# Kernel optimization log

Hardware: AMD Instinct MI355X
Metric: run time of the kernel (lower is better)

The kernel has to match this reference:

```python
import jax, jax.numpy as jnp
import numpy as np

N_NODES = 50000
K_MAX = 10
BATCH = 64
T = 32
N_INPUTS = 16
BITS_PER_FEATURE = 4
INPUT_BITS = N_INPUTS * BITS_PER_FEATURE  # 64


def setup_inputs() -> dict:
    key = jax.random.key(0)
    ks = jax.random.split(key, 8)
    x = jax.random.randint(ks[0], (BATCH, T, INPUT_BITS), 0, 2, dtype=jnp.int32)
    adj_list = jax.random.randint(ks[1], (N_NODES, K_MAX), 0, N_NODES, dtype=jnp.int32)
    adj_list_mask = jax.random.randint(ks[2], (N_NODES, K_MAX), 0, 2, dtype=jnp.int32)
    lut = jax.random.randint(ks[3], (N_NODES, 2 ** K_MAX), 0, 2, dtype=jnp.int32)
    init_states = jax.random.randint(ks[4], (N_NODES,), 0, 2, dtype=jnp.int32)
    input_nodes = jax.random.randint(ks[5], (INPUT_BITS,), 0, N_NODES, dtype=jnp.int32)
    W = jax.random.normal(ks[6], (N_INPUTS, N_NODES), dtype=jnp.float32) * (1.0 / np.sqrt(N_NODES))
    b = jax.random.normal(ks[7], (N_INPUTS,), dtype=jnp.float32) * 0.01
    return {"x": x, "adj_list": adj_list, "adj_list_mask": adj_list_mask,
            "lut": lut, "init_states": init_states, "input_nodes": input_nodes,
            "W": W, "b": b}


def reference(x, adj_list, adj_list_mask, lut, init_states, input_nodes, W, b):
    B, T_, _ = x.shape
    N, K = adj_list.shape
    # powers_of_2 = 2**arange(K).flip()  (MSB-first bit packing)
    pow2 = (2 ** jnp.arange(K - 1, -1, -1)).astype(jnp.int32)  # [K]
    node_ids = jnp.arange(N, dtype=jnp.int32)  # [N]
    s0 = jnp.broadcast_to(init_states[None, :], (B, N)).astype(jnp.int32)

    def step(states, x_t):
        # xor input perturbation at input_nodes
        cur = states[:, input_nodes]                      # [B, INPUT_BITS]
        states = states.at[:, input_nodes].set(jnp.bitwise_xor(cur, x_t))
        # gather masked neighbor states and bit-pack into LUT index
        neigh = jnp.take(states, adj_list, axis=1)        # [B, N, K]
        idx = jnp.sum(neigh * adj_list_mask[None] * pow2, axis=-1)  # [B, N]
        new_states = lut[node_ids[None, :], idx]          # [B, N]
        return new_states, None

    final_states, _ = jax.lax.scan(step, s0, jnp.moveaxis(x, 1, 0))
    # readout = nn.Linear(n_nodes, n_inputs) on final binary states
    out = final_states.astype(jnp.float32) @ W.T + b      # [B, N_INPUTS]
    return out
```

## Files before the change

### kernel.cpp

```cpp
#include <hip/hip_runtime.h>
#include <stdint.h>

#define N_NODES    50000
#define K_MAX      10
#define BATCH      64
#define T_STEPS    32
#define N_INPUTS   16
#define INPUT_BITS 64

#define NPW   256
#define NWG   196
#define NTHR  1024

#define OFF_BUF0   0u
#define OFF_BUF1   400128u
#define OFF_XMASK  800256u
#define OFF_CTR    816640u

__global__ void prep_kernel(const int* __restrict__ x,
                            const int* __restrict__ init_states,
                            const int* __restrict__ input_nodes,
                            uint64_t* __restrict__ buf0,
                            uint64_t* __restrict__ buf1,
                            uint64_t* __restrict__ xmask,
                            uint32_t* __restrict__ ctr) {
    int gid = blockIdx.x * blockDim.x + threadIdx.x;
    if (gid < N_NODES) {
        int n = gid;
        int jm = -1;
        for (int j = 0; j < INPUT_BITS; ++j)
            if (input_nodes[j] == n) jm = j;
        uint64_t v = init_states[n] ? ~0ull : 0ull;
        if (jm >= 0) {
            uint64_t m = 0ull;
            for (int b = 0; b < BATCH; ++b)
                m |= (uint64_t)(x[b * (T_STEPS * INPUT_BITS) + jm] & 1) << b;
            v ^= m;
        }
        buf0[n] = v;
    } else if (gid == N_NODES) {
        buf0[N_NODES] = 0ull; buf1[N_NODES] = 0ull;
    } else if (gid < N_NODES + 1 + T_STEPS * INPUT_BITS) {
        int k = gid - (N_NODES + 1);
        int t = k >> 6, j = k & 63;
        uint64_t m = 0ull;
        for (int b = 0; b < BATCH; ++b)
            m |= (uint64_t)(x[b * (T_STEPS * INPUT_BITS) + t * INPUT_BITS + j] & 1) << b;
        xmask[k] = m;
    } else {
        int c = gid - (N_NODES + 1 + T_STEPS * INPUT_BITS);
        if (c < T_STEPS) ctr[c] = 0;
    }
}

__global__ __launch_bounds__(NTHR)
void reservoir_coop(const int* __restrict__ adj,
                    const int* __restrict__ adjmask,
                    const int* __restrict__ lut,
                    const int* __restrict__ input_nodes,
                    const uint64_t* __restrict__ xmask,
                    uint64_t* __restrict__ buf0,
                    uint64_t* __restrict__ buf1,
                    uint32_t* __restrict__ ctr) {
    __shared__ uint8_t lutb[NPW * 128];

    const int tid  = threadIdx.x;
    const int lane = tid & 63;
    const int wv   = tid >> 6;
    const int wg   = blockIdx.x;

    for (int rr = 0; rr < 16; ++rr) {
        int r  = wv * 16 + rr;
        int gn = wg * NPW + r;
        if (gn < N_NODES) {
            uint64_t mine = 0ull;
            #pragma unroll
            for (int c = 0; c < 16; ++c) {
                int v = lut[(size_t)gn * 1024 + (size_t)c * 64 + lane];
                uint64_t m = __ballot(v & 1);
                if (lane == c) mine = m;
            }
            if (lane < 16) ((uint64_t*)lutb)[r * 16 + lane] = mine;
        }
    }

    const int nl   = tid >> 2;
    const int q    = tid & 3;
    const int node = wg * NPW + nl;
    const bool valid = node < N_NODES;
    const uint32_t qsh = (uint32_t)(q & 1) * 16;

    uint32_t off[K_MAX];
    uint32_t soff = 0;
    int jm = -1;
    if (valid) {
        #pragma unroll
        for (int k = 0; k < K_MAX; ++k) {
            int a  = adj[node * K_MAX + k];
            int mk = adjmask[node * K_MAX + k];
            off[k] = (uint32_t)(mk ? a : N_NODES) * 8u + (uint32_t)(q >> 1) * 4u;
        }
        for (int j = 0; j < INPUT_BITS; ++j)
            if (input_nodes[j] == node) jm = j;
        soff = (uint32_t)node * 8u + (uint32_t)(q >> 1) * 4u;
    }
    const int rowbase = nl * 128;
    __syncthreads();

    uint64_t* cur = buf0;
    uint64_t* nxt = buf1;

    for (int t = 0; t < T_STEPS; ++t) {
        if (valid) {
            const char* src = (const char*)cur;
            uint32_t w[K_MAX];
            #pragma unroll
            for (int k = 0; k < K_MAX; ++k)
                w[k] = __hip_atomic_load((const uint32_t*)(src + off[k]),
                                         __ATOMIC_RELAXED, __HIP_MEMORY_SCOPE_AGENT) >> qsh;

            uint32_t o16 = 0;
            #pragma unroll
            for (int b = 0; b < 16; ++b) {
                uint32_t idx = 0;
                #pragma unroll
                for (int k = 0; k < K_MAX; ++k)
                    idx = (idx << 1) | ((w[k] >> b) & 1u);
                uint32_t d = *(const uint32_t*)(lutb + rowbase + ((idx >> 5) << 2));
                o16 |= ((d >> (idx & 31)) & 1u) << b;
            }

            uint32_t hi = __shfl_down(o16, 1);
            if ((q & 1) == 0) {
                uint32_t o32 = o16 | (hi << 16);
                if (jm >= 0 && t < T_STEPS - 1)
                    o32 ^= ((const uint32_t*)xmask)[((t + 1) * INPUT_BITS + jm) * 2 + (q >> 1)];
                __hip_atomic_store((uint32_t*)((char*)nxt + soff), o32,
                                   __ATOMIC_RELAXED, __HIP_MEMORY_SCOPE_AGENT);
            }
        }

        __syncthreads();
        if (tid == 0) {
            __hip_atomic_fetch_add(&ctr[t], 1u, __ATOMIC_RELAXED, __HIP_MEMORY_SCOPE_AGENT);
            while (__hip_atomic_load(&ctr[t], __ATOMIC_RELAXED, __HIP_MEMORY_SCOPE_AGENT) < (uint32_t)NWG)
                __builtin_amdgcn_s_sleep(2);
        }
        __syncthreads();
        asm volatile("" ::: "memory");

        uint64_t* tmp = cur; cur = nxt; nxt = tmp;
    }
}

__global__ void out_kernel(const uint64_t* __restrict__ fstate,
                           const float* __restrict__ W,
                           const float* __restrict__ bias,
                           float* __restrict__ out) {
    const int wg = blockIdx.x;
    const int b = wg >> 4, i = wg & 15;
    const int tid = threadIdx.x;
    const uint8_t* st = (const uint8_t*)fstate;
    const int byteoff = b >> 3, bsh = b & 7;

    float s = 0.f;
    for (int n = tid; n < N_NODES; n += 256) {
        uint32_t bit = (st[(size_t)n * 8 + byteoff] >> bsh) & 1u;
        s += (float)bit * W[(size_t)i * N_NODES + n];
    }
    #pragma unroll
    for (int off = 32; off; off >>= 1) s += __shfl_down(s, off);

    __shared__ float part[4];
    const int lane = tid & 63, wave = tid >> 6;
    if (lane == 0) part[wave] = s;
    __syncthreads();
    if (tid == 0) out[wg] = part[0] + part[1] + part[2] + part[3] + bias[i];
}

extern "C" void kernel_launch(void* const* d_in, const int* in_sizes, int n_in,
                              void* d_out, int out_size, void* d_ws, size_t ws_size,
                              hipStream_t stream) {
    const int*   x       = (const int*)d_in[0];
    const int*   adj     = (const int*)d_in[1];
    const int*   adjmask = (const int*)d_in[2];
    const int*   lut     = (const int*)d_in[3];
    const int*   initst  = (const int*)d_in[4];
    const int*   innodes = (const int*)d_in[5];
    const float* W       = (const float*)d_in[6];
    const float* bias    = (const float*)d_in[7];
    float* out = (float*)d_out;

    char* ws = (char*)d_ws;
    uint64_t* buf0  = (uint64_t*)(ws + OFF_BUF0);
    uint64_t* buf1  = (uint64_t*)(ws + OFF_BUF1);
    uint64_t* xmask = (uint64_t*)(ws + OFF_XMASK);
    uint32_t* ctr   = (uint32_t*)(ws + OFF_CTR);

    {
        int prep_threads = (N_NODES + 1) + T_STEPS * INPUT_BITS + T_STEPS;
        int prep_blocks = (prep_threads + 255) / 256;
        hipLaunchKernelGGL(prep_kernel, dim3(prep_blocks), dim3(256), 0, stream,
                           x, initst, innodes, buf0, buf1, xmask, ctr);
    }

    {
        void* args[] = { (void*)&adj, (void*)&adjmask, (void*)&lut, (void*)&innodes,
                         (void*)&xmask, (void*)&buf0, (void*)&buf1, (void*)&ctr };
        hipLaunchCooperativeKernel((void*)reservoir_coop,
                                   dim3(NWG), dim3(NTHR),
                                   args, 0, stream);
    }

    hipLaunchKernelGGL(out_kernel, dim3(BATCH * N_INPUTS), dim3(256), 0, stream,
                       (const uint64_t*)buf0, W, bias, out);
}
```

Measured before the change: 403.5 us.

## Pack LUT in a separate kernel and use per-step state buffers

LUT bit-packing moves out of the cooperative kernel into its own fully parallel kernel, one block per node. The cooperative kernel then copies each workgroup's packed 32 KB slice straight into LDS. The two ping-pong state buffers become T+1 distinct buffers, one per step. Each address is written once before it is read, so the neighbor gathers can use plain loads instead of agent-scope atomic loads, and the final grid barrier is dropped. This costs about 13 MB of extra workspace, an extra launch, and a 200 MB packing pass that now runs as a standalone kernel.

```diff
diff --git a/kernel.cpp b/kernel.cpp
--- a/kernel.cpp
+++ b/kernel.cpp
@@ -11,20 +11,23 @@
 #define NPW   256
 #define NWG   196
 #define NTHR  1024
-
-#define OFF_BUF0   0u
-#define OFF_BUF1   400128u
-#define OFF_XMASK  800256u
-#define OFF_CTR    816640u
+#define NBUF  (T_STEPS + 1)
+
+#define BUF_STRIDE_B 400128u
+
+#define OFF_BUFS   0u
+#define OFF_XMASK  (NBUF * BUF_STRIDE_B)
+#define OFF_CTR    (OFF_XMASK + 16384u)
+#define OFF_PLUT   (OFF_CTR + 128u)
 
 __global__ void prep_kernel(const int* __restrict__ x,
                             const int* __restrict__ init_states,
                             const int* __restrict__ input_nodes,
-                            uint64_t* __restrict__ buf0,
-                            uint64_t* __restrict__ buf1,
+                            uint64_t* __restrict__ bufs,
                             uint64_t* __restrict__ xmask,
                             uint32_t* __restrict__ ctr) {
-    int gid = blockIdx.x * blockDim.x + threadIdx.x;
+    const int gid = blockIdx.x * blockDim.x + threadIdx.x;
+    const size_t strw = BUF_STRIDE_B / 8;
     if (gid < N_NODES) {
         int n = gid;
         int jm = -1;
@@ -37,51 +40,49 @@
                 m |= (uint64_t)(x[b * (T_STEPS * INPUT_BITS) + jm] & 1) << b;
             v ^= m;
         }
-        buf0[n] = v;
-    } else if (gid == N_NODES) {
-        buf0[N_NODES] = 0ull; buf1[N_NODES] = 0ull;
-    } else if (gid < N_NODES + 1 + T_STEPS * INPUT_BITS) {
-        int k = gid - (N_NODES + 1);
+        bufs[n] = v;
+    } else if (gid < N_NODES + NBUF) {
+        bufs[(size_t)(gid - N_NODES) * strw + N_NODES] = 0ull;
+    } else if (gid < N_NODES + NBUF + T_STEPS * INPUT_BITS) {
+        int k = gid - (N_NODES + NBUF);
         int t = k >> 6, j = k & 63;
         uint64_t m = 0ull;
         for (int b = 0; b < BATCH; ++b)
             m |= (uint64_t)(x[b * (T_STEPS * INPUT_BITS) + t * INPUT_BITS + j] & 1) << b;
         xmask[k] = m;
-    } else {
-        int c = gid - (N_NODES + 1 + T_STEPS * INPUT_BITS);
-        if (c < T_STEPS) ctr[c] = 0;
-    }
+    } else if (gid < N_NODES + NBUF + T_STEPS * INPUT_BITS + T_STEPS) {
+        ctr[gid - (N_NODES + NBUF + T_STEPS * INPUT_BITS)] = 0;
+    }
+}
+
+__global__ void lutpack_kernel(const int* __restrict__ lut,
+                               uint64_t* __restrict__ plut) {
+    const int tid = threadIdx.x;
+    const int blk = blockIdx.x;
+    const int lane = tid & 63, wave = tid >> 6;
+    int v = lut[(size_t)blk * 1024 + tid];
+    uint64_t m = __ballot(v & 1);
+    if (lane == 0) plut[(size_t)blk * 16 + wave] = m;
 }
 
 __global__ __launch_bounds__(NTHR)
-void reservoir_coop(const int* __restrict__ adj,
+void reservoir_coop(const uint64_t* __restrict__ plut,
+                    const int* __restrict__ adj,
                     const int* __restrict__ adjmask,
-                    const int* __restrict__ lut,
                     const int* __restrict__ input_nodes,
                     const uint64_t* __restrict__ xmask,
-                    uint64_t* __restrict__ buf0,
-                    uint64_t* __restrict__ buf1,
+                    uint64_t* __restrict__ bufs,
                     uint32_t* __restrict__ ctr) {
     __shared__ uint8_t lutb[NPW * 128];
 
-    const int tid  = threadIdx.x;
-    const int lane = tid & 63;
-    const int wv   = tid >> 6;
-    const int wg   = blockIdx.x;
-
-    for (int rr = 0; rr < 16; ++rr) {
-        int r  = wv * 16 + rr;
-        int gn = wg * NPW + r;
-        if (gn < N_NODES) {
-            uint64_t mine = 0ull;
-            #pragma unroll
-            for (int c = 0; c < 16; ++c) {
-                int v = lut[(size_t)gn * 1024 + (size_t)c * 64 + lane];
-                uint64_t m = __ballot(v & 1);
-                if (lane == c) mine = m;
-            }
-            if (lane < 16) ((uint64_t*)lutb)[r * 16 + lane] = mine;
-        }
+    const int tid = threadIdx.x;
+    const int wg  = blockIdx.x;
+
+    {
+        const uint4* src = (const uint4*)(plut + (size_t)wg * NPW * 16);
+        uint4* dst = (uint4*)lutb;
+        dst[tid * 2]     = src[tid * 2];
+        dst[tid * 2 + 1] = src[tid * 2 + 1];
     }
 
     const int nl   = tid >> 2;
@@ -107,17 +108,14 @@
     const int rowbase = nl * 128;
     __syncthreads();
 
-    uint64_t* cur = buf0;
-    uint64_t* nxt = buf1;
-
     for (int t = 0; t < T_STEPS; ++t) {
+        const char* src = (const char*)bufs + (size_t)t * BUF_STRIDE_B;
+        char*       dst = (char*)bufs + (size_t)(t + 1) * BUF_STRIDE_B;
         if (valid) {
-            const char* src = (const char*)cur;
             uint32_t w[K_MAX];
             #pragma unroll
             for (int k = 0; k < K_MAX; ++k)
-                w[k] = __hip_atomic_load((const uint32_t*)(src + off[k]),
-                                         __ATOMIC_RELAXED, __HIP_MEMORY_SCOPE_AGENT) >> qsh;
+                w[k] = *(const uint32_t*)(src + off[k]) >> qsh;
 
             uint32_t o16 = 0;
             #pragma unroll
@@ -135,21 +133,21 @@
                 uint32_t o32 = o16 | (hi << 16);
                 if (jm >= 0 && t < T_STEPS - 1)
                     o32 ^= ((const uint32_t*)xmask)[((t + 1) * INPUT_BITS + jm) * 2 + (q >> 1)];
-                __hip_atomic_store((uint32_t*)((char*)nxt + soff), o32,
+                __hip_atomic_store((uint32_t*)(dst + soff), o32,
                                    __ATOMIC_RELAXED, __HIP_MEMORY_SCOPE_AGENT);
             }
         }
 
-        __syncthreads();
-        if (tid == 0) {
-            __hip_atomic_fetch_add(&ctr[t], 1u, __ATOMIC_RELAXED, __HIP_MEMORY_SCOPE_AGENT);
-            while (__hip_atomic_load(&ctr[t], __ATOMIC_RELAXED, __HIP_MEMORY_SCOPE_AGENT) < (uint32_t)NWG)
-                __builtin_amdgcn_s_sleep(2);
-        }
-        __syncthreads();
-        asm volatile("" ::: "memory");
-
-        uint64_t* tmp = cur; cur = nxt; nxt = tmp;
+        if (t < T_STEPS - 1) {
+            __syncthreads();
+            if (tid == 0) {
+                __hip_atomic_fetch_add(&ctr[t], 1u, __ATOMIC_RELAXED, __HIP_MEMORY_SCOPE_AGENT);
+                while (__hip_atomic_load(&ctr[t], __ATOMIC_RELAXED, __HIP_MEMORY_SCOPE_AGENT)
+                       < (uint32_t)NWG)
+                    __builtin_amdgcn_s_sleep(2);
+            }
+            __syncthreads();
+        }
     }
 }
 
@@ -192,26 +190,29 @@
     float* out = (float*)d_out;
 
     char* ws = (char*)d_ws;
-    uint64_t* buf0  = (uint64_t*)(ws + OFF_BUF0);
-    uint64_t* buf1  = (uint64_t*)(ws + OFF_BUF1);
+    uint64_t* bufs  = (uint64_t*)(ws + OFF_BUFS);
     uint64_t* xmask = (uint64_t*)(ws + OFF_XMASK);
     uint32_t* ctr   = (uint32_t*)(ws + OFF_CTR);
+    uint64_t* plut  = (uint64_t*)(ws + OFF_PLUT);
 
     {
-        int prep_threads = (N_NODES + 1) + T_STEPS * INPUT_BITS + T_STEPS;
+        int prep_threads = N_NODES + NBUF + T_STEPS * INPUT_BITS + T_STEPS;
         int prep_blocks = (prep_threads + 255) / 256;
         hipLaunchKernelGGL(prep_kernel, dim3(prep_blocks), dim3(256), 0, stream,
-                           x, initst, innodes, buf0, buf1, xmask, ctr);
-    }
+                           x, initst, innodes, bufs, xmask, ctr);
+    }
+
+    hipLaunchKernelGGL(lutpack_kernel, dim3(N_NODES), dim3(1024), 0, stream, lut, plut);
 
     {
-        void* args[] = { (void*)&adj, (void*)&adjmask, (void*)&lut, (void*)&innodes,
-                         (void*)&xmask, (void*)&buf0, (void*)&buf1, (void*)&ctr };
+        void* args[] = { (void*)&plut, (void*)&adj, (void*)&adjmask, (void*)&innodes,
+                         (void*)&xmask, (void*)&bufs, (void*)&ctr };
         hipLaunchCooperativeKernel((void*)reservoir_coop,
                                    dim3(NWG), dim3(NTHR),
                                    args, 0, stream);
     }
 
     hipLaunchKernelGGL(out_kernel, dim3(BATCH * N_INPUTS), dim3(256), 0, stream,
-                       (const uint64_t*)buf0, W, bias, out);
-}
+                       (const uint64_t*)(ws + OFF_BUFS + (size_t)T_STEPS * BUF_STRIDE_B),
+                       W, bias, out);
+}
```

New measurement: 388.8 us. 3.7% less time.
